# Performance work log

Hardware: AMD Instinct MI355X
Metric: run time of the kernel (lower is better)

Reference implementation:

```python
import jax, jax.numpy as jnp
import numpy as np

def setup_inputs() -> dict:
    key = jax.random.key(0)
    ks = jax.random.split(key, 6)
    B, H, Dk, Dv = 128, 16, 128, 128
    return {
        "q": jax.random.normal(ks[0], (B, H, 1, Dk), dtype=jnp.float32),
        "k": jax.random.normal(ks[1], (B, H, 1, Dk), dtype=jnp.float32),
        "v": jax.random.normal(ks[2], (B, H, 1, Dv), dtype=jnp.float32),
        "g": jax.random.uniform(ks[3], (B, H, 1), dtype=jnp.float32),
        "beta": jax.random.uniform(ks[4], (B, H, 1), dtype=jnp.float32),
        "last_recurrent_state": jax.random.normal(ks[5], (B, H, Dk, Dv), dtype=jnp.float32),
    }

def reference(q, k, v, g, beta, last_recurrent_state):
    # q,k: (B,H,1,Dk); v: (B,H,1,Dv); g,beta: (B,H,1); state: (B,H,Dk,Dv)
    q_t = q[:, :, 0, :]                      # (B,H,Dk)
    k_t = k[:, :, 0, :]                      # (B,H,Dk)
    v_t = v[:, :, 0, :]                      # (B,H,Dv)
    decay = jnp.exp(g)[..., None]            # (B,H,1,1)
    state = last_recurrent_state * decay     # (B,H,Dk,Dv)
    kv_mem = jnp.einsum('bhkv,bhk->bhv', state, k_t)   # (B,H,Dv)
    delta = (v_t - kv_mem) * beta            # (B,H,Dv)
    state = state + k_t[..., :, None] * delta[..., None, :]  # outer update
    out = jnp.einsum('bhkv,bhk->bhv', state, q_t)       # (B,H,Dv)
    out = out[:, :, None, :]                 # (B,H,1,Dv)
    return jnp.concatenate([out.reshape(-1), state.reshape(-1)], axis=0)
```

## Files before the change

### kernel.cpp

```cpp
#include <hip/hip_runtime.h>
#include <hip/hip_bf16.h>


#define DK 128
#define DV 128

__global__ __launch_bounds__(256, 4) void s1_cell_kernel(
    const float* __restrict__ q,
    const float* __restrict__ k,
    const float* __restrict__ v,
    const float* __restrict__ g,
    const float* __restrict__ beta,
    const float* __restrict__ S,
    float* __restrict__ out,
    int BH)
{
    const int bh = blockIdx.x;
    const size_t stile = (size_t)bh * DK * DV;
    const float* __restrict__ Sb   = S + stile;
    float* __restrict__ out_o      = out + (size_t)bh * DV;
    float* __restrict__ out_S      = out + (size_t)BH * DV + stile;

    __shared__ float kt[DK];
    __shared__ float qt[DK];
    __shared__ float vt[DV];
    __shared__ float apart[8][DV];
    __shared__ float bpart[8][DV];
    __shared__ float sdelta[DV];
    __shared__ float s_kq;

    const int t = threadIdx.x;
    const int vb = (t & 31) * 4;
    const int kb = (t >> 5) * 16;
    const int grp = t >> 5;

    if (t < DK) {
        kt[t] = k[bh * DK + t];
        qt[t] = q[bh * DK + t];
        vt[t] = v[bh * DV + t];
    }

    float4 s[16];
    const float* __restrict__ base = Sb + (size_t)kb * DV + vb;
    #pragma unroll
    for (int i = 0; i < 16; ++i)
        s[i] = *(const float4*)(base + (size_t)i * DV);

    const float decay = expf(g[bh]);
    const float bta   = beta[bh];

    __syncthreads();

    float a0 = 0.f, a1 = 0.f, a2 = 0.f, a3 = 0.f;
    float b0 = 0.f, b1 = 0.f, b2 = 0.f, b3 = 0.f;
    #pragma unroll
    for (int i = 0; i < 16; ++i) {
        const float kv = kt[kb + i];
        const float qv = qt[kb + i];
        a0 += s[i].x * kv;  a1 += s[i].y * kv;  a2 += s[i].z * kv;  a3 += s[i].w * kv;
        b0 += s[i].x * qv;  b1 += s[i].y * qv;  b2 += s[i].z * qv;  b3 += s[i].w * qv;
    }
    apart[grp][vb + 0] = a0;  apart[grp][vb + 1] = a1;
    apart[grp][vb + 2] = a2;  apart[grp][vb + 3] = a3;
    bpart[grp][vb + 0] = b0;  bpart[grp][vb + 1] = b1;
    bpart[grp][vb + 2] = b2;  bpart[grp][vb + 3] = b3;

    if (t < 64) {
        float val = kt[t] * qt[t] + kt[t + 64] * qt[t + 64];
        #pragma unroll
        for (int off = 32; off > 0; off >>= 1)
            val += __shfl_down(val, off, 64);
        if (t == 0) s_kq = val;
    }
    __syncthreads();

    if (t < DV) {
        float A = 0.f, Bq = 0.f;
        #pragma unroll
        for (int j = 0; j < 8; ++j) {
            A  += apart[j][t];
            Bq += bpart[j][t];
        }
        const float dlt = (vt[t] - decay * A) * bta;
        sdelta[t] = dlt;
        out_o[t] = decay * Bq + s_kq * dlt;
    }
    __syncthreads();

    const float d0 = sdelta[vb + 0];
    const float d1 = sdelta[vb + 1];
    const float d2 = sdelta[vb + 2];
    const float d3 = sdelta[vb + 3];

    float* __restrict__ obase = out_S + (size_t)kb * DV + vb;
    #pragma unroll
    for (int i = 0; i < 16; ++i) {
        const float ktk = kt[kb + i];
        float4 r;
        r.x = decay * s[i].x + ktk * d0;
        r.y = decay * s[i].y + ktk * d1;
        r.z = decay * s[i].z + ktk * d2;
        r.w = decay * s[i].w + ktk * d3;
        *(float4*)(obase + (size_t)i * DV) = r;
    }
}

extern "C" void kernel_launch(void* const* d_in, const int* in_sizes, int n_in,
                              void* d_out, int out_size, void* d_ws, size_t ws_size,
                              hipStream_t stream) {
    const float* q    = (const float*)d_in[0];
    const float* k    = (const float*)d_in[1];
    const float* v    = (const float*)d_in[2];
    const float* g    = (const float*)d_in[3];
    const float* beta = (const float*)d_in[4];
    const float* S    = (const float*)d_in[5];
    float* out = (float*)d_out;

    const int BH = in_sizes[3];

    s1_cell_kernel<<<BH, 256, 0, stream>>>(q, k, v, g, beta, S, out, BH);
}
```

Before: 249.2 us.

## Reduce state matvecs within each wavefront via shuffles, removing shared memory and barriers

```diff
diff --git a/kernel.cpp b/kernel.cpp
--- a/kernel.cpp
+++ b/kernel.cpp
@@ -16,92 +16,104 @@
     int BH)
 {
     const int bh = blockIdx.x;
+    const int t  = threadIdx.x;
+    const int w  = t >> 6;
+    const int l  = t & 63;
+    const int kg = l >> 2;
+    const int vg = l & 3;
+    const int vb = w * 32 + vg * 8;
+    const int kb = kg * 8;
+
     const size_t stile = (size_t)bh * DK * DV;
-    const float* __restrict__ Sb   = S + stile;
-    float* __restrict__ out_o      = out + (size_t)bh * DV;
-    float* __restrict__ out_S      = out + (size_t)BH * DV + stile;
+    const float* __restrict__ Sb = S + stile + (size_t)kb * DV + vb;
+    float* __restrict__ So       = out + (size_t)BH * DV + stile + (size_t)kb * DV + vb;
+    float* __restrict__ out_o    = out + (size_t)bh * DV;
 
-    __shared__ float kt[DK];
-    __shared__ float qt[DK];
-    __shared__ float vt[DV];
-    __shared__ float apart[8][DV];
-    __shared__ float bpart[8][DV];
-    __shared__ float sdelta[DV];
-    __shared__ float s_kq;
+    const float4* kp = (const float4*)(k + bh * DK + kb);
+    const float4* qp = (const float4*)(q + bh * DK + kb);
+    const float4* vp = (const float4*)(v + bh * DV + vb);
 
-    const int t = threadIdx.x;
-    const int vb = (t & 31) * 4;
-    const int kb = (t >> 5) * 16;
-    const int grp = t >> 5;
-
-    if (t < DK) {
-        kt[t] = k[bh * DK + t];
-        qt[t] = q[bh * DK + t];
-        vt[t] = v[bh * DV + t];
+    float4 s0[8], s1[8];
+    #pragma unroll
+    for (int i = 0; i < 8; ++i) {
+        s0[i] = *(const float4*)(Sb + (size_t)i * DV);
+        s1[i] = *(const float4*)(Sb + (size_t)i * DV + 4);
     }
 
-    float4 s[16];
-    const float* __restrict__ base = Sb + (size_t)kb * DV + vb;
-    #pragma unroll
-    for (int i = 0; i < 16; ++i)
-        s[i] = *(const float4*)(base + (size_t)i * DV);
+    float4 kA = kp[0], kB = kp[1];
+    float4 qA = qp[0], qB = qp[1];
+    float kr[8] = {kA.x, kA.y, kA.z, kA.w, kB.x, kB.y, kB.z, kB.w};
+    float qr[8] = {qA.x, qA.y, qA.z, qA.w, qB.x, qB.y, qB.z, qB.w};
 
     const float decay = expf(g[bh]);
     const float bta   = beta[bh];
 
-    __syncthreads();
+    float a[8] = {0,0,0,0,0,0,0,0};
+    float b[8] = {0,0,0,0,0,0,0,0};
+    float kq = 0.f;
+    #pragma unroll
+    for (int i = 0; i < 8; ++i) {
+        const float kv = kr[i], qv = qr[i];
+        a[0] += s0[i].x * kv; a[1] += s0[i].y * kv;
+        a[2] += s0[i].z * kv; a[3] += s0[i].w * kv;
+        a[4] += s1[i].x * kv; a[5] += s1[i].y * kv;
+        a[6] += s1[i].z * kv; a[7] += s1[i].w * kv;
+        b[0] += s0[i].x * qv; b[1] += s0[i].y * qv;
+        b[2] += s0[i].z * qv; b[3] += s0[i].w * qv;
+        b[4] += s1[i].x * qv; b[5] += s1[i].y * qv;
+        b[6] += s1[i].z * qv; b[7] += s1[i].w * qv;
+        kq   += kv * qv;
+    }
 
-    float a0 = 0.f, a1 = 0.f, a2 = 0.f, a3 = 0.f;
-    float b0 = 0.f, b1 = 0.f, b2 = 0.f, b3 = 0.f;
     #pragma unroll
-    for (int i = 0; i < 16; ++i) {
-        const float kv = kt[kb + i];
-        const float qv = qt[kb + i];
-        a0 += s[i].x * kv;  a1 += s[i].y * kv;  a2 += s[i].z * kv;  a3 += s[i].w * kv;
-        b0 += s[i].x * qv;  b1 += s[i].y * qv;  b2 += s[i].z * qv;  b3 += s[i].w * qv;
-    }
-    apart[grp][vb + 0] = a0;  apart[grp][vb + 1] = a1;
-    apart[grp][vb + 2] = a2;  apart[grp][vb + 3] = a3;
-    bpart[grp][vb + 0] = b0;  bpart[grp][vb + 1] = b1;
-    bpart[grp][vb + 2] = b2;  bpart[grp][vb + 3] = b3;
-
-    if (t < 64) {
-        float val = kt[t] * qt[t] + kt[t + 64] * qt[t + 64];
-        #pragma unroll
-        for (int off = 32; off > 0; off >>= 1)
-            val += __shfl_down(val, off, 64);
-        if (t == 0) s_kq = val;
-    }
-    __syncthreads();
-
-    if (t < DV) {
-        float A = 0.f, Bq = 0.f;
+    for (int m = 4; m <= 32; m <<= 1) {
         #pragma unroll
         for (int j = 0; j < 8; ++j) {
-            A  += apart[j][t];
-            Bq += bpart[j][t];
+            a[j] += __shfl_xor(a[j], m, 64);
+            b[j] += __shfl_xor(b[j], m, 64);
         }
-        const float dlt = (vt[t] - decay * A) * bta;
-        sdelta[t] = dlt;
-        out_o[t] = decay * Bq + s_kq * dlt;
+        kq += __shfl_xor(kq, m, 64);
     }
-    __syncthreads();
 
-    const float d0 = sdelta[vb + 0];
-    const float d1 = sdelta[vb + 1];
-    const float d2 = sdelta[vb + 2];
-    const float d3 = sdelta[vb + 3];
+    float4 v0 = vp[0], v1 = vp[1];
+    float d[8];
+    d[0] = (v0.x - decay * a[0]) * bta;
+    d[1] = (v0.y - decay * a[1]) * bta;
+    d[2] = (v0.z - decay * a[2]) * bta;
+    d[3] = (v0.w - decay * a[3]) * bta;
+    d[4] = (v1.x - decay * a[4]) * bta;
+    d[5] = (v1.y - decay * a[5]) * bta;
+    d[6] = (v1.z - decay * a[6]) * bta;
+    d[7] = (v1.w - decay * a[7]) * bta;
 
-    float* __restrict__ obase = out_S + (size_t)kb * DV + vb;
+    if (kg == 0) {
+        float4 o0, o1;
+        o0.x = decay * b[0] + kq * d[0];
+        o0.y = decay * b[1] + kq * d[1];
+        o0.z = decay * b[2] + kq * d[2];
+        o0.w = decay * b[3] + kq * d[3];
+        o1.x = decay * b[4] + kq * d[4];
+        o1.y = decay * b[5] + kq * d[5];
+        o1.z = decay * b[6] + kq * d[6];
+        o1.w = decay * b[7] + kq * d[7];
+        *(float4*)(out_o + vb)     = o0;
+        *(float4*)(out_o + vb + 4) = o1;
+    }
+
     #pragma unroll
-    for (int i = 0; i < 16; ++i) {
-        const float ktk = kt[kb + i];
-        float4 r;
-        r.x = decay * s[i].x + ktk * d0;
-        r.y = decay * s[i].y + ktk * d1;
-        r.z = decay * s[i].z + ktk * d2;
-        r.w = decay * s[i].w + ktk * d3;
-        *(float4*)(obase + (size_t)i * DV) = r;
+    for (int i = 0; i < 8; ++i) {
+        const float kv = kr[i];
+        float4 r0, r1;
+        r0.x = decay * s0[i].x + kv * d[0];
+        r0.y = decay * s0[i].y + kv * d[1];
+        r0.z = decay * s0[i].z + kv * d[2];
+        r0.w = decay * s0[i].w + kv * d[3];
+        r1.x = decay * s1[i].x + kv * d[4];
+        r1.y = decay * s1[i].y + kv * d[5];
+        r1.z = decay * s1[i].z + kv * d[6];
+        r1.w = decay * s1[i].w + kv * d[7];
+        *(float4*)(So + (size_t)i * DV)     = r0;
+        *(float4*)(So + (size_t)i * DV + 4) = r1;
     }
 }
 
```

New measurement: 253.3 us. About the same (+1.6%).
